# Performance work log

Measured on AMD Instinct MI355X. Metric: run time of the kernel, lower is better.

Reference implementation:

```python
import jax, jax.numpy as jnp
import numpy as np

B, S, HID, NH, NS = 2, 1024, 2048, 16, 8
D = HID // NH  # head_dim = 128


def setup_inputs() -> dict:
    key = jax.random.key(0)
    ks = jax.random.split(key, 8)
    inv = 1.0 / np.sqrt(HID)
    return {
        "hidden_states": jax.random.normal(ks[0], (B, S, HID), jnp.float32),
        "Wq": jax.random.normal(ks[1], (HID, HID), jnp.float32) * inv,
        "Wk": jax.random.normal(ks[2], (HID, HID), jnp.float32) * inv,
        "Wv": jax.random.normal(ks[3], (HID, HID), jnp.float32) * inv,
        "Wo": jax.random.normal(ks[4], (HID, HID), jnp.float32) * inv,
        "splat_positions": jax.random.normal(ks[5], (NH, NS, D), jnp.float32) * 0.02,
        "splat_directions": jax.random.normal(ks[6], (NH, NS, D), jnp.float32) * 0.02,
        "splat_log_scales": jnp.full((NH, NS), np.log(0.8), jnp.float32),
        "splat_log_amplitudes": jnp.full((NH, NS), -np.log(float(NS)), jnp.float32),
        "directional_strength": jnp.float32(0.3),
        "gsa_strength": jnp.float32(-6.0),
    }


def _affinities(tokens, positions, directions, scales, dir_strength):
    # tokens [B,NH,S,D]; positions/directions [NH,NS,D]; scales [NH,NS]
    tok_sq = jnp.sum(tokens * tokens, axis=-1)                       # [B,NH,S]
    pos_sq = jnp.sum(positions * positions, axis=-1)                 # [NH,NS]
    tp = jnp.einsum('bhsd,hnd->bhsn', tokens, positions)             # [B,NH,S,NS]
    dist2 = tok_sq[..., None] - 2.0 * tp + pos_sq[None, :, None, :]
    dist2 = jnp.maximum(dist2, 0.0)
    # signed projection of (token - position) onto unit direction
    proj = (jnp.einsum('bhsd,hnd->bhsn', tokens, directions)
            - jnp.sum(positions * directions, axis=-1)[None, :, None, :])
    perp2 = jnp.maximum(dist2 - proj * proj, 0.0)
    inv2s2 = (0.5 / (scales * scales))[None, :, None, :]
    radial = jnp.exp(-dist2 * inv2s2)
    directional = jnp.exp(-perp2 * inv2s2)
    return (1.0 - dir_strength) * radial + dir_strength * directional


def reference(hidden_states, Wq, Wk, Wv, Wo, splat_positions, splat_directions,
              splat_log_scales, splat_log_amplitudes, directional_strength, gsa_strength):
    b, s, hid = hidden_states.shape

    def heads(x):  # [B,S,HID] -> [B,NH,S,D]
        return x.reshape(b, s, NH, D).transpose(0, 2, 1, 3)

    q = heads(hidden_states @ Wq)
    k = heads(hidden_states @ Wk)
    v = heads(hidden_states @ Wv)

    # --- standard (original) attention path ---
    scores = jnp.einsum('bhqd,bhkd->bhqk', q, k) / jnp.sqrt(jnp.float32(D))
    attn = jax.nn.softmax(scores, axis=-1)
    std = jnp.einsum('bhqk,bhkd->bhqd', attn, v)
    std = std.transpose(0, 2, 1, 3).reshape(b, s, hid) @ Wo

    # --- directional GSA path ---
    eps = 1e-12
    positions = splat_positions / (jnp.linalg.norm(splat_positions, axis=-1, keepdims=True) + eps)
    positions = positions * (np.sqrt(D) * 0.3)
    directions = splat_directions / (jnp.linalg.norm(splat_directions, axis=-1, keepdims=True) + eps)
    scales = jnp.clip(jnp.exp(splat_log_scales), 0.3, 1.2)
    amplitudes = jax.nn.softmax(splat_log_amplitudes, axis=-1)
    ds = jax.nn.sigmoid(directional_strength)

    qa = _affinities(q, positions, directions, scales, ds)  # [B,NH,S,NS]
    ka = _affinities(k, positions, directions, scales, ds)  # [B,NH,S,NS]
    w = jnp.einsum('bhqn,hn,bhkn->bhqk', qa, amplitudes, ka)
    w = w / (jnp.sum(w, axis=-1, keepdims=True) + 1e-8)
    dgsa = jnp.einsum('bhqk,bhkd->bhqd', w, v)
    dgsa = dgsa.transpose(0, 2, 1, 3).reshape(b, s, hid) @ Wo

    gsa = jax.nn.sigmoid(gsa_strength)
    blend = jnp.minimum(0.05, gsa * 0.1)
    return (1.0 - blend) * std + blend * dgsa
```

## Files before the change

kernel.cpp:

```cpp
#include <hip/hip_runtime.h>
#include <math.h>

typedef __attribute__((ext_vector_type(8))) short bf16x8;
typedef __attribute__((ext_vector_type(4))) float f32x4;
typedef unsigned short ushort_t;

#define SQRT_D 11.313708498984761f
#define INV_SQRT_D 0.08838834764831845f

__device__ __forceinline__ unsigned short f2b(float f) {
    unsigned u = __float_as_uint(f);
    unsigned r = (u + 0x7fffu + ((u >> 16) & 1u)) >> 16;
    return (unsigned short)r;
}
__device__ __forceinline__ float b2f(unsigned short h) {
    return __uint_as_float(((unsigned)h) << 16);
}

__device__ __forceinline__ void async_copy16(const void* g, void* l) {
    __builtin_amdgcn_global_load_lds((const __attribute__((address_space(1))) void*)g,
                                     (__attribute__((address_space(3))) void*)l, 16, 0, 0);
}

__global__ __launch_bounds__(256) void prep(
    const float* __restrict__ X, const float* __restrict__ W0,
    const float* __restrict__ W1, const float* __restrict__ W2,
    const float* __restrict__ W3, const float* __restrict__ sp,
    const float* __restrict__ sd, const float* __restrict__ ls,
    const float* __restrict__ la, ushort_t* __restrict__ Xbf,
    ushort_t* __restrict__ WT4, float* __restrict__ posn,
    float* __restrict__ dirn, float* __restrict__ pos_sq,
    float* __restrict__ pdv, float* __restrict__ iv2s2,
    float* __restrict__ amp) {
    __shared__ float t[32][33];
    const int z = blockIdx.z;
    if (z < 4) {
        const float* W = (z == 0) ? W0 : (z == 1) ? W1 : (z == 2) ? W2 : W3;
        ushort_t* WT = WT4 + (size_t)z * 4194304;
        int tx = threadIdx.x & 31, ty = threadIdx.x >> 5;
        int bn = blockIdx.x * 32, bk = blockIdx.y * 32;
#pragma unroll
        for (int i = 0; i < 4; ++i)
            t[ty + i * 8][tx] = W[(size_t)(bk + ty + i * 8) * 2048 + bn + tx];
        __syncthreads();
#pragma unroll
        for (int i = 0; i < 4; ++i)
            WT[(size_t)(bn + ty + i * 8) * 2048 + bk + tx] = f2b(t[tx][ty + i * 8]);
        return;
    }
    {
        int bi = blockIdx.y * 64 + blockIdx.x;
        int i = (bi * 256 + threadIdx.x) * 4;
        float4 v = *(const float4*)(X + i);
        ushort4 o;
        o.x = f2b(v.x); o.y = f2b(v.y); o.z = f2b(v.z); o.w = f2b(v.w);
        *(ushort4*)(Xbf + i) = o;
    }
    if (blockIdx.x == 0 && blockIdx.y == 0 && threadIdx.x < 128) {
        int i = threadIdx.x;
        const float* p = sp + (size_t)i * 128;
        const float* d = sd + (size_t)i * 128;
        float np_ = 0.f, nd_ = 0.f;
        for (int k = 0; k < 128; ++k) { np_ += p[k] * p[k]; nd_ += d[k] * d[k]; }
        np_ = sqrtf(np_); nd_ = sqrtf(nd_);
        const float sc = 3.394112549695428f;
        float rp = sc / (np_ + 1e-12f);
        float rd = 1.f / (nd_ + 1e-12f);
        float psq = 0.f, pd_ = 0.f;
        for (int k = 0; k < 128; ++k) {
            float pn = p[k] * rp;
            float dn = d[k] * rd;
            posn[(size_t)i * 128 + k] = pn;
            dirn[(size_t)i * 128 + k] = dn;
            psq += pn * pn;
            pd_ += pn * dn;
        }
        pos_sq[i] = psq;
        pdv[i] = pd_;
        float s = expf(ls[i]);
        s = fminf(fmaxf(s, 0.3f), 1.2f);
        iv2s2[i] = 0.5f / (s * s);
        if ((i & 7) == 0) {
            int h = i >> 3;
            float mx = -INFINITY;
            for (int n = 0; n < 8; ++n) mx = fmaxf(mx, la[h * 8 + n]);
            float e[8]; float ssum = 0.f;
            for (int n = 0; n < 8; ++n) { e[n] = expf(la[h * 8 + n] - mx); ssum += e[n]; }
            for (int n = 0; n < 8; ++n) amp[h * 8 + n] = e[n] / ssum;
        }
    }
}


__global__ __launch_bounds__(256) void gemm_qkv(const ushort_t* __restrict__ A,
                                                const ushort_t* __restrict__ WT4,
                                                ushort_t* __restrict__ Qb,
                                                ushort_t* __restrict__ Kb,
                                                ushort_t* __restrict__ Vb,
                                                ushort_t* __restrict__ Vt) {
    __shared__ ushort_t As0[128 * 32], As1[128 * 32];
    __shared__ ushort_t Bs0[128 * 32], Bs1[128 * 32];
    const int tid = threadIdx.x, lane = tid & 63, wave = tid >> 6;
    const int l15 = lane & 15, quad = lane >> 4;
    const int wm = (wave >> 1) * 64, wn = (wave & 1) * 64;
    const int bm = blockIdx.x * 128;
    const int by = blockIdx.y, which = by >> 4, bn = (by & 15) * 128;
    const ushort_t* BT = WT4 + (size_t)which * 4194304;
    f32x4 acc[4][4] = {};
    const int off0 = tid * 16;
    const int row0 = tid >> 2;
    const int c0 = (tid & 3) ^ ((row0 + (row0 >> 2)) & 3);
    const ushort_t* ga = A + (size_t)(bm + row0) * 2048 + c0 * 8;
    const ushort_t* gb = BT + (size_t)(bn + row0) * 2048 + c0 * 8;
    const int rsw = (l15 + (l15 >> 2)) & 3;
#define STAGEG(ABUF, BBUF, k_)                                                 \
    {                                                                          \
        async_copy16(ga + (k_), (char*)(ABUF) + off0);                         \
        async_copy16(ga + (size_t)64 * 2048 + (k_), (char*)(ABUF) + off0 + 4096); \
        async_copy16(gb + (k_), (char*)(BBUF) + off0);                         \
        async_copy16(gb + (size_t)64 * 2048 + (k_), (char*)(BBUF) + off0 + 4096); \
    }
#define COMPUTEG(ABUF, BBUF)                                                   \
    {                                                                          \
        bf16x8 af[4], bfr[4];                                                  \
        _Pragma("unroll") for (int i = 0; i < 4; ++i)                          \
            af[i] = *(const bf16x8*)((const char*)(ABUF) + (wm + i * 16 + l15) * 64 + ((quad ^ rsw) << 4)); \
        _Pragma("unroll") for (int j = 0; j < 4; ++j)                          \
            bfr[j] = *(const bf16x8*)((const char*)(BBUF) + (wn + j * 16 + l15) * 64 + ((quad ^ rsw) << 4)); \
        _Pragma("unroll") for (int i = 0; i < 4; ++i)                          \
            _Pragma("unroll") for (int j = 0; j < 4; ++j)                      \
                acc[i][j] = __builtin_amdgcn_mfma_f32_16x16x32_bf16(af[i], bfr[j], acc[i][j], 0, 0, 0); \
    }
    STAGEG(As0, Bs0, 0);
    for (int k0 = 0; k0 < 2048; k0 += 64) {
        __syncthreads();
        STAGEG(As1, Bs1, k0 + 32);
        COMPUTEG(As0, Bs0);
        __syncthreads();
        if (k0 + 64 < 2048) STAGEG(As0, Bs0, k0 + 64);
        COMPUTEG(As1, Bs1);
    }
#undef STAGEG
#undef COMPUTEG
    ushort_t* Cb = (which == 0) ? Qb : ((which == 1) ? Kb : Vb);
    const bool dot = (which == 2);
    const float oscale = (which == 0) ? INV_SQRT_D : 1.f;
#pragma unroll
    for (int i = 0; i < 4; ++i) {
#pragma unroll
        for (int j = 0; j < 4; ++j) {
            int m0 = bm + wm + i * 16 + quad * 4;
            int n = bn + wn + j * 16 + l15;
            int b = m0 >> 10, s0 = m0 & 1023, h = n >> 7, d = n & 127;
            ushort4 pack;
            unsigned short* pp = (unsigned short*)&pack;
#pragma unroll
            for (int r = 0; r < 4; ++r) {
                unsigned short bv = f2b(acc[i][j][r] * oscale);
                pp[r] = bv;
                Cb[((size_t)((b << 4) | h) * 1024 + (s0 + r)) * 128 + d] = bv;
            }
            if (dot) *(ushort4*)(Vt + ((size_t)((b << 4) | h) * 128 + d) * 1024 + s0) = pack;
        }
    }
}

__global__ __launch_bounds__(256) void gemm_out(const ushort_t* __restrict__ A,
                                                const ushort_t* __restrict__ BT,
                                                float* __restrict__ Cf) {
    __shared__ ushort_t As0[128 * 32], As1[128 * 32];
    __shared__ ushort_t Bs0[64 * 32], Bs1[64 * 32];
    const int tid = threadIdx.x, lane = tid & 63, wave = tid >> 6;
    const int l15 = lane & 15, quad = lane >> 4;
    const int wm = (wave >> 1) * 64, wn = (wave & 1) * 32;
    const int bm = blockIdx.x * 128, bn = blockIdx.y * 64;
    f32x4 acc[4][2] = {};
    const int off0 = tid * 16;
    const int row0 = tid >> 2;
    const int c0 = (tid & 3) ^ ((row0 + (row0 >> 2)) & 3);
    const ushort_t* ga = A + (size_t)(bm + row0) * 2048 + c0 * 8;
    const ushort_t* gb = BT + (size_t)(bn + row0) * 2048 + c0 * 8;
    const int rsw = (l15 + (l15 >> 2)) & 3;
#define STAGEO(ABUF, BBUF, k_)                                                 \
    {                                                                          \
        async_copy16(ga + (k_), (char*)(ABUF) + off0);                         \
        async_copy16(ga + (size_t)64 * 2048 + (k_), (char*)(ABUF) + off0 + 4096); \
        async_copy16(gb + (k_), (char*)(BBUF) + off0);                         \
    }
#define COMPUTEO(ABUF, BBUF)                                                   \
    {                                                                          \
        bf16x8 af[4], bfr[2];                                                  \
        _Pragma("unroll") for (int i = 0; i < 4; ++i)                          \
            af[i] = *(const bf16x8*)((const char*)(ABUF) + (wm + i * 16 + l15) * 64 + ((quad ^ rsw) << 4)); \
        _Pragma("unroll") for (int j = 0; j < 2; ++j)                          \
            bfr[j] = *(const bf16x8*)((const char*)(BBUF) + (wn + j * 16 + l15) * 64 + ((quad ^ rsw) << 4)); \
        _Pragma("unroll") for (int i = 0; i < 4; ++i)                          \
            _Pragma("unroll") for (int j = 0; j < 2; ++j)                      \
                acc[i][j] = __builtin_amdgcn_mfma_f32_16x16x32_bf16(af[i], bfr[j], acc[i][j], 0, 0, 0); \
    }
    STAGEO(As0, Bs0, 0);
    for (int k0 = 0; k0 < 2048; k0 += 64) {
        __syncthreads();
        STAGEO(As1, Bs1, k0 + 32);
        COMPUTEO(As0, Bs0);
        __syncthreads();
        if (k0 + 64 < 2048) STAGEO(As0, Bs0, k0 + 64);
        COMPUTEO(As1, Bs1);
    }
#undef STAGEO
#undef COMPUTEO
#pragma unroll
    for (int i = 0; i < 4; ++i)
#pragma unroll
        for (int j = 0; j < 2; ++j)
#pragma unroll
            for (int r = 0; r < 4; ++r) {
                int m = bm + wm + i * 16 + quad * 4 + r;
                int n = bn + wn + j * 16 + l15;
                Cf[(size_t)m * 2048 + n] = acc[i][j][r];
            }
}

__global__ __launch_bounds__(256) void affinity_q(
    const ushort_t* __restrict__ Q,
    const float* __restrict__ posn, const float* __restrict__ dirn,
    const float* __restrict__ pos_sq, const float* __restrict__ pdv,
    const float* __restrict__ iv2s2, const float* __restrict__ ds_in,
    float* __restrict__ qa) {
    int gid = blockIdx.x * 256 + threadIdx.x;
    int n = gid & 7;
    int t = gid >> 3;
    const ushort_t* T = Q + (size_t)t * 128;
    int h = (t >> 10) & 15;
    const float* P = posn + (size_t)(h * 8 + n) * 128;
    const float* Dr = dirn + (size_t)(h * 8 + n) * 128;
    float tsq = 0.f, tp = 0.f, td = 0.f;
#pragma unroll
    for (int d = 0; d < 128; d += 8) {
        uint4 raw = *(const uint4*)(T + d);
        float tv[8];
        tv[0] = __uint_as_float(raw.x << 16); tv[1] = __uint_as_float(raw.x & 0xffff0000u);
        tv[2] = __uint_as_float(raw.y << 16); tv[3] = __uint_as_float(raw.y & 0xffff0000u);
        tv[4] = __uint_as_float(raw.z << 16); tv[5] = __uint_as_float(raw.z & 0xffff0000u);
        tv[6] = __uint_as_float(raw.w << 16); tv[7] = __uint_as_float(raw.w & 0xffff0000u);
        float4 p0 = *(const float4*)(P + d), p1 = *(const float4*)(P + d + 4);
        float4 d0 = *(const float4*)(Dr + d), d1 = *(const float4*)(Dr + d + 4);
        tsq += tv[0]*tv[0]+tv[1]*tv[1]+tv[2]*tv[2]+tv[3]*tv[3]+tv[4]*tv[4]+tv[5]*tv[5]+tv[6]*tv[6]+tv[7]*tv[7];
        tp  += tv[0]*p0.x+tv[1]*p0.y+tv[2]*p0.z+tv[3]*p0.w+tv[4]*p1.x+tv[5]*p1.y+tv[6]*p1.z+tv[7]*p1.w;
        td  += tv[0]*d0.x+tv[1]*d0.y+tv[2]*d0.z+tv[3]*d0.w+tv[4]*d1.x+tv[5]*d1.y+tv[6]*d1.z+tv[7]*d1.w;
    }
    const float fs = SQRT_D;
    tsq *= fs * fs; tp *= fs; td *= fs;
    float dist2 = fmaxf(tsq - 2.f * tp + pos_sq[h * 8 + n], 0.f);
    float proj = td - pdv[h * 8 + n];
    float perp2 = fmaxf(dist2 - proj * proj, 0.f);
    float iv = iv2s2[h * 8 + n];
    float dsv = 1.f / (1.f + __expf(-ds_in[0]));
    float aff = (1.f - dsv) * __expf(-dist2 * iv) + dsv * __expf(-perp2 * iv);
    qa[(size_t)t * 8 + n] = aff;
}

__global__ __launch_bounds__(128) void kv_s1_part(
    const ushort_t* __restrict__ K, const ushort_t* __restrict__ V,
    const float* __restrict__ posn, const float* __restrict__ dirn,
    const float* __restrict__ pos_sq, const float* __restrict__ pdv,
    const float* __restrict__ iv2s2, const float* __restrict__ ds_in,
    float* __restrict__ KVp, float* __restrict__ S1p) {
    __shared__ float kas[64][8];
    int bh = blockIdx.x, sc = blockIdx.y;
    int tid = threadIdx.x;
    int h = bh & 15;
    if (tid < 64) {
        const ushort_t* T = K + ((size_t)bh * 1024 + sc * 64 + tid) * 128;
        float tsq = 0.f, tp[8] = {}, td[8] = {};
        for (int d = 0; d < 128; d += 4) {
            uint2 raw = *(const uint2*)(T + d);
            float t0 = __uint_as_float(raw.x << 16), t1 = __uint_as_float(raw.x & 0xffff0000u);
            float t2 = __uint_as_float(raw.y << 16), t3 = __uint_as_float(raw.y & 0xffff0000u);
            tsq += t0 * t0 + t1 * t1 + t2 * t2 + t3 * t3;
#pragma unroll
            for (int n = 0; n < 8; ++n) {
                const float* P = posn + (size_t)(h * 8 + n) * 128 + d;
                const float* Dr = dirn + (size_t)(h * 8 + n) * 128 + d;
                tp[n] += t0 * P[0] + t1 * P[1] + t2 * P[2] + t3 * P[3];
                td[n] += t0 * Dr[0] + t1 * Dr[1] + t2 * Dr[2] + t3 * Dr[3];
            }
        }
        float dsv = 1.f / (1.f + __expf(-ds_in[0]));
#pragma unroll
        for (int n = 0; n < 8; ++n) {
            float dist2 = fmaxf(tsq - 2.f * tp[n] + pos_sq[h * 8 + n], 0.f);
            float proj = td[n] - pdv[h * 8 + n];
            float perp2 = fmaxf(dist2 - proj * proj, 0.f);
            float iv = iv2s2[h * 8 + n];
            kas[tid][n] = (1.f - dsv) * __expf(-dist2 * iv) + dsv * __expf(-perp2 * iv);
        }
    }
    __syncthreads();
    int d = tid;
    const ushort_t* VB = V + ((size_t)bh * 1024 + sc * 64) * 128;
    float acc[8] = {};
#pragma unroll 4
    for (int s = 0; s < 64; ++s) {
        float vd = b2f(VB[(size_t)s * 128 + d]);
#pragma unroll
        for (int n = 0; n < 8; ++n) acc[n] += kas[s][n] * vd;
    }
#pragma unroll
    for (int n = 0; n < 8; ++n) KVp[(((size_t)bh * 8 + n) * 16 + sc) * 128 + d] = acc[n];
    __shared__ float s1p[128];
    {
        int n = d >> 4, chunk = d & 15;
        float p = 0.f;
        for (int s = chunk * 4; s < chunk * 4 + 4; ++s) p += kas[s][n];
        s1p[d] = p;
    }
    __syncthreads();
    if (d < 8) {
        float t = 0.f;
        for (int c = 0; c < 16; ++c) t += s1p[(d << 4) + c];
        S1p[((size_t)bh * 8 + d) * 16 + sc] = t;
    }
}

__global__ __launch_bounds__(256) void flash_blend(
    const ushort_t* __restrict__ Qg, const ushort_t* __restrict__ Kg,
    const ushort_t* __restrict__ Vtg,
    const float* __restrict__ qa, const float* __restrict__ amp,
    const float* __restrict__ S1p, const float* __restrict__ KVp,
    const float* __restrict__ gstr, ushort_t* __restrict__ blended) {
    __shared__ ushort_t Ks0[64 * 128], Ks1[64 * 128];
    __shared__ ushort_t Vt0[128 * 64], Vt1[128 * 64];
    __shared__ ushort_t Ps[4][16 * 72];
    __shared__ float KVs[8 * 128];
    __shared__ float S1s[8];
    const int tid = threadIdx.x, lane = tid & 63, wave = tid >> 6;
    const int l15 = lane & 15, quad = lane >> 4;
    const int bh = blockIdx.y, qt = blockIdx.x;

    const ushort_t* Qrow = Qg + ((size_t)(bh * 1024 + qt * 64 + wave * 16 + l15)) * 128 + quad * 8;
    bf16x8 aq[4];
#pragma unroll
    for (int k4 = 0; k4 < 4; ++k4) aq[k4] = *(const bf16x8*)(Qrow + k4 * 32);

    {
        int n = tid >> 5, d = (tid & 31) * 4;
        f32x4 kv = {};
#pragma unroll
        for (int sc = 0; sc < 16; ++sc)
            kv += *(const f32x4*)(KVp + (((size_t)bh * 8 + n) * 16 + sc) * 128 + d);
        *(f32x4*)(KVs + tid * 4) = kv;
    }
    if (tid < 8) {
        float s = 0.f;
#pragma unroll
        for (int sc = 0; sc < 16; ++sc) s += S1p[((size_t)bh * 8 + tid) * 16 + sc];
        S1s[tid] = s;
    }

    const ushort_t* Kbase = Kg + (size_t)bh * 131072;
    const ushort_t* Vbase = Vtg + (size_t)bh * 131072;

#define STAGE(KBUF, VBUF, kt_)                                                        \
    {                                                                                 \
        _Pragma("unroll") for (int i_ = 0; i_ < 4; ++i_) {                            \
            int off_ = tid * 16 + i_ * 4096;                                          \
            int kr_ = off_ >> 8, kp_ = (off_ >> 4) & 15;                              \
            async_copy16(Kbase + (size_t)(kt_)*8192 + kr_ * 128 + ((kp_ ^ (kr_ & 15)) << 3), \
                         (char*)(KBUF) + off_);                                       \
            int vd_ = off_ >> 7, vp_ = (off_ >> 4) & 7;                               \
            async_copy16(Vbase + (size_t)vd_ * 1024 + (kt_)*64 + ((vp_ ^ (vd_ & 7)) << 3), \
                         (char*)(VBUF) + off_);                                       \
        }                                                                             \
    }
#define FLASH_STEP(KBUF, VBUF)                                                        \
    {                                                                                 \
        f32x4 sc[4] = {};                                                             \
        _Pragma("unroll") for (int k4 = 0; k4 < 4; ++k4) {                            \
            _Pragma("unroll") for (int t = 0; t < 4; ++t) {                           \
                bf16x8 bk = *(const bf16x8*)((const char*)(KBUF) +                    \
                                             ((t * 16 + l15) << 8) + (((k4 * 4 + quad) ^ l15) << 4)); \
                sc[t] = __builtin_amdgcn_mfma_f32_16x16x32_bf16(aq[k4], bk, sc[t], 0, 0, 0); \
            }                                                                         \
        }                                                                             \
        _Pragma("unroll") for (int t = 0; t < 4; ++t) {                               \
            _Pragma("unroll") for (int r = 0; r < 4; ++r) {                           \
                float p = __expf(sc[t][r]);                                           \
                l_i[r] += p;                                                          \
                Pw[(quad * 4 + r) * 72 + t * 16 + l15] = f2b(p);                      \
            }                                                                         \
        }                                                                             \
        bf16x8 ap0 = *(const bf16x8*)((const char*)Pw + (l15 * 72 + quad * 8) * 2);   \
        bf16x8 ap1 = *(const bf16x8*)((const char*)Pw + (l15 * 72 + 32 + quad * 8) * 2); \
        _Pragma("unroll") for (int j = 0; j < 8; ++j) {                               \
            bf16x8 bv0 = *(const bf16x8*)((const char*)(VBUF) +                       \
                                          ((j * 16 + l15) << 7) + (((quad) ^ (l15 & 7)) << 4)); \
            bf16x8 bv1 = *(const bf16x8*)((const char*)(VBUF) +                       \
                                          ((j * 16 + l15) << 7) + (((4 + quad) ^ (l15 & 7)) << 4)); \
            o[j] = __builtin_amdgcn_mfma_f32_16x16x32_bf16(ap0, bv0, o[j], 0, 0, 0);  \
            o[j] = __builtin_amdgcn_mfma_f32_16x16x32_bf16(ap1, bv1, o[j], 0, 0, 0);  \
        }                                                                             \
    }

    STAGE(Ks0, Vt0, 0);

    f32x4 o[8] = {};
    float l_i[4] = {};
    ushort_t* Pw = &Ps[wave][0];

    for (int kt = 0; kt < 16; kt += 2) {
        __syncthreads();
        STAGE(Ks1, Vt1, kt + 1);
        FLASH_STEP(Ks0, Vt0);
        __syncthreads();
        if (kt + 2 < 16) STAGE(Ks0, Vt0, kt + 2);
        FLASH_STEP(Ks1, Vt1);
    }
#undef STAGE
#undef FLASH_STEP
#pragma unroll
    for (int r = 0; r < 4; ++r) {
        float l = l_i[r];
        l += __shfl_xor(l, 1);
        l += __shfl_xor(l, 2);
        l += __shfl_xor(l, 4);
        l += __shfl_xor(l, 8);
        l_i[r] = l;
    }
    float gsa = 1.f / (1.f + __expf(-gstr[0]));
    float blend = fminf(0.05f, gsa * 0.1f);
    int b = bh >> 4, h = bh & 15;
#pragma unroll
    for (int r = 0; r < 4; ++r) {
        int q = qt * 64 + wave * 16 + quad * 4 + r;
        const float* qaRow = qa + ((size_t)bh * 1024 + q) * 8;
        float qam[8], Z = 0.f;
#pragma unroll
        for (int n = 0; n < 8; ++n) {
            qam[n] = qaRow[n] * amp[h * 8 + n];
            Z += qam[n] * S1s[n];
        }
        float invZ = 1.f / (Z + 1e-8f);
        float invl = 1.f / l_i[r];
        ushort_t* outp = blended + ((size_t)(b * 1024 + q)) * 2048 + h * 128;
#pragma unroll
        for (int j = 0; j < 8; ++j) {
            int d = j * 16 + l15;
            float dg = 0.f;
#pragma unroll
            for (int n = 0; n < 8; ++n) dg += qam[n] * KVs[n * 128 + d];
            float v = (1.f - blend) * (o[j][r] * invl) + blend * (dg * invZ);
            outp[d] = f2b(v);
        }
    }
}

extern "C" void kernel_launch(void* const* d_in, const int* in_sizes, int n_in,
                              void* d_out, int out_size, void* d_ws, size_t ws_size,
                              hipStream_t stream) {
    const float* X = (const float*)d_in[0];
    const float* Wq = (const float*)d_in[1];
    const float* Wk = (const float*)d_in[2];
    const float* Wv = (const float*)d_in[3];
    const float* Wo = (const float*)d_in[4];
    const float* sp = (const float*)d_in[5];
    const float* sd = (const float*)d_in[6];
    const float* ls = (const float*)d_in[7];
    const float* la = (const float*)d_in[8];
    const float* dstr = (const float*)d_in[9];
    const float* gstr = (const float*)d_in[10];

    char* base = (char*)d_ws;
    ushort_t* WT4 = (ushort_t*)base;      base += 33554432;
    ushort_t* Xbf = (ushort_t*)base;      base += 8388608;
    ushort_t* blended = Xbf;
    ushort_t* Qbf = (ushort_t*)base;      base += 8388608;
    ushort_t* Kbf = (ushort_t*)base;      base += 8388608;
    ushort_t* Vbf = (ushort_t*)base;      base += 8388608;
    ushort_t* Vtb = (ushort_t*)base;      base += 8388608;
    float* qaw = (float*)base;            base += 1048576;
    float* posn = (float*)base;           base += 65536;
    float* dirn = (float*)base;           base += 65536;
    float* pos_sq = (float*)base;         base += 512;
    float* pdv = (float*)base;            base += 512;
    float* iv2s2 = (float*)base;          base += 512;
    float* ampw = (float*)base;           base += 512;
    float* S1p = (float*)base;            base += 16384;
    float* KVp = (float*)base;            base += 2097152;

    prep<<<dim3(64, 64, 5), 256, 0, stream>>>(X, Wq, Wk, Wv, Wo, sp, sd, ls, la,
                                              Xbf, WT4, posn, dirn, pos_sq, pdv, iv2s2, ampw);
    gemm_qkv<<<dim3(16, 48), 256, 0, stream>>>(Xbf, WT4, Qbf, Kbf, Vbf, Vtb);
    affinity_q<<<1024, 256, 0, stream>>>(Qbf, posn, dirn, pos_sq, pdv, iv2s2, dstr, qaw);
    kv_s1_part<<<dim3(32, 16), 128, 0, stream>>>(Kbf, Vbf, posn, dirn, pos_sq, pdv, iv2s2,
                                                 dstr, KVp, S1p);
    flash_blend<<<dim3(16, 32), 256, 0, stream>>>(Qbf, Kbf, Vtb, qaw, ampw, S1p, KVp,
                                                  gstr, blended);
    gemm_out<<<dim3(16, 32), 256, 0, stream>>>(blended, WT4 + 12582912, (float*)d_out);
}
```

Baseline: 332.5 us.

## Restructure QKV GEMM into 256x256 tiles with four-stage async LDS pipeline

The QKV projection GEMM moves from 128x128 tiles with 256 threads and double buffering to 256x256 tiles with 512 threads (8 waves). It uses a four-slot LDS ring fed by async global-to-LDS loads, with explicit vmcnt waits, raw s_barrier, sched_barrier and setprio around the MFMA bursts. The larger tile raises arithmetic intensity per LDS byte and the deeper pipeline is meant to hide global load latency. In exchange it uses 128KB of LDS and a larger accumulator footprint. It also launches only 192 blocks, which may underfill the GPU.

```diff
diff --git a/kernel.cpp b/kernel.cpp
--- a/kernel.cpp
+++ b/kernel.cpp
@@ -92,75 +92,136 @@
 }
 
 
-__global__ __launch_bounds__(256) void gemm_qkv(const ushort_t* __restrict__ A,
-                                                const ushort_t* __restrict__ WT4,
-                                                ushort_t* __restrict__ Qb,
-                                                ushort_t* __restrict__ Kb,
-                                                ushort_t* __restrict__ Vb,
-                                                ushort_t* __restrict__ Vt) {
-    __shared__ ushort_t As0[128 * 32], As1[128 * 32];
-    __shared__ ushort_t Bs0[128 * 32], Bs1[128 * 32];
+__global__ __launch_bounds__(512, 2) void gemm_qkv(const ushort_t* __restrict__ A,
+                                                   const ushort_t* __restrict__ WT4,
+                                                   ushort_t* __restrict__ Qb,
+                                                   ushort_t* __restrict__ Kb,
+                                                   ushort_t* __restrict__ Vb,
+                                                   ushort_t* __restrict__ Vt) {
+    __shared__ ushort_t Asl[4 * 8192];
+    __shared__ ushort_t Bsl[4 * 8192];
     const int tid = threadIdx.x, lane = tid & 63, wave = tid >> 6;
     const int l15 = lane & 15, quad = lane >> 4;
-    const int wm = (wave >> 1) * 64, wn = (wave & 1) * 64;
-    const int bm = blockIdx.x * 128;
-    const int by = blockIdx.y, which = by >> 4, bn = (by & 15) * 128;
+    const int wr = wave >> 2, wc = wave & 3;
+    const int wm = wr * 128, wn = wc * 64;
+    const int bm = blockIdx.x * 256;
+    const int by = blockIdx.y, which = by >> 3, bn = (by & 7) * 256;
     const ushort_t* BT = WT4 + (size_t)which * 4194304;
-    f32x4 acc[4][4] = {};
-    const int off0 = tid * 16;
-    const int row0 = tid >> 2;
-    const int c0 = (tid & 3) ^ ((row0 + (row0 >> 2)) & 3);
-    const ushort_t* ga = A + (size_t)(bm + row0) * 2048 + c0 * 8;
-    const ushort_t* gb = BT + (size_t)(bn + row0) * 2048 + c0 * 8;
+    f32x4 acc[8][4] = {};
+    const int srow = tid >> 2;
+    const int sc = tid & 3;
+    const int swz0 = (srow + (srow >> 2)) & 3;
+    const ushort_t* gA = A + (size_t)(bm + srow) * 2048 + (sc ^ swz0) * 8;
+    const ushort_t* gB = BT + (size_t)(bn + srow) * 2048 + (sc ^ swz0) * 8;
+    char* ldsA = (char*)Asl + tid * 16;
+    char* ldsB = (char*)Bsl + tid * 16;
     const int rsw = (l15 + (l15 >> 2)) & 3;
-#define STAGEG(ABUF, BBUF, k_)                                                 \
+    const int cxo = (quad ^ rsw) << 4;
+    bf16x8 bfr[4];
+
+#define STAGE_A(slot, kofs)                                                    \
     {                                                                          \
-        async_copy16(ga + (k_), (char*)(ABUF) + off0);                         \
-        async_copy16(ga + (size_t)64 * 2048 + (k_), (char*)(ABUF) + off0 + 4096); \
-        async_copy16(gb + (k_), (char*)(BBUF) + off0);                         \
-        async_copy16(gb + (size_t)64 * 2048 + (k_), (char*)(BBUF) + off0 + 4096); \
-    }
-#define COMPUTEG(ABUF, BBUF)                                                   \
+        char* db_ = ldsA + (slot) * 16384;                                     \
+        async_copy16(gA + (kofs), db_);                                        \
+        async_copy16(gA + 262144 + (kofs), db_ + 8192);                        \
+    }
+#define STAGE_B(slot, kofs)                                                    \
     {                                                                          \
-        bf16x8 af[4], bfr[4];                                                  \
+        char* db_ = ldsB + (slot) * 16384;                                     \
+        async_copy16(gB + (kofs), db_);                                        \
+        async_copy16(gB + 262144 + (kofs), db_ + 8192);                        \
+    }
+#define VMW(n) asm volatile("s_waitcnt vmcnt(" #n ")" ::: "memory")
+#define PHA(sa, ISSUE, WAIT)                                                   \
+    {                                                                          \
+        const char* Ab_ = (const char*)Asl + (sa) * 16384;                     \
+        const char* Bb_ = (const char*)Bsl + (sa) * 16384;                     \
+        bf16x8 af[4];                                                          \
         _Pragma("unroll") for (int i = 0; i < 4; ++i)                          \
-            af[i] = *(const bf16x8*)((const char*)(ABUF) + (wm + i * 16 + l15) * 64 + ((quad ^ rsw) << 4)); \
+            af[i] = *(const bf16x8*)(Ab_ + (wm + i * 16 + l15) * 64 + cxo);    \
         _Pragma("unroll") for (int j = 0; j < 4; ++j)                          \
-            bfr[j] = *(const bf16x8*)((const char*)(BBUF) + (wn + j * 16 + l15) * 64 + ((quad ^ rsw) << 4)); \
+            bfr[j] = *(const bf16x8*)(Bb_ + (wn + j * 16 + l15) * 64 + cxo);   \
+        ISSUE;                                                                 \
+        WAIT;                                                                  \
+        __builtin_amdgcn_s_barrier();                                          \
+        asm volatile("s_waitcnt lgkmcnt(0)" ::: "memory");                     \
+        __builtin_amdgcn_sched_barrier(0);                                     \
+        __builtin_amdgcn_s_setprio(1);                                         \
         _Pragma("unroll") for (int i = 0; i < 4; ++i)                          \
             _Pragma("unroll") for (int j = 0; j < 4; ++j)                      \
                 acc[i][j] = __builtin_amdgcn_mfma_f32_16x16x32_bf16(af[i], bfr[j], acc[i][j], 0, 0, 0); \
-    }
-    STAGEG(As0, Bs0, 0);
-    for (int k0 = 0; k0 < 2048; k0 += 64) {
-        __syncthreads();
-        STAGEG(As1, Bs1, k0 + 32);
-        COMPUTEG(As0, Bs0);
-        __syncthreads();
-        if (k0 + 64 < 2048) STAGEG(As0, Bs0, k0 + 64);
-        COMPUTEG(As1, Bs1);
-    }
-#undef STAGEG
-#undef COMPUTEG
+        __builtin_amdgcn_s_setprio(0);                                         \
+        __builtin_amdgcn_s_barrier();                                          \
+    }
+#define PHB(sa, ISSUE, WAIT)                                                   \
+    {                                                                          \
+        const char* Ab_ = (const char*)Asl + (sa) * 16384;                     \
+        bf16x8 af[4];                                                          \
+        _Pragma("unroll") for (int i = 0; i < 4; ++i)                          \
+            af[i] = *(const bf16x8*)(Ab_ + (wm + (i + 4) * 16 + l15) * 64 + cxo); \
+        ISSUE;                                                                 \
+        WAIT;                                                                  \
+        __builtin_amdgcn_s_barrier();                                          \
+        asm volatile("s_waitcnt lgkmcnt(0)" ::: "memory");                     \
+        __builtin_amdgcn_sched_barrier(0);                                     \
+        __builtin_amdgcn_s_setprio(1);                                         \
+        _Pragma("unroll") for (int i = 0; i < 4; ++i)                          \
+            _Pragma("unroll") for (int j = 0; j < 4; ++j)                      \
+                acc[i + 4][j] = __builtin_amdgcn_mfma_f32_16x16x32_bf16(af[i], bfr[j], acc[i + 4][j], 0, 0, 0); \
+        __builtin_amdgcn_s_setprio(0);                                         \
+        __builtin_amdgcn_s_barrier();                                          \
+    }
+
+    STAGE_A(0, 0);
+    STAGE_B(0, 0);
+    STAGE_A(1, 32);
+    STAGE_B(1, 32);
+    STAGE_A(2, 64);
+    STAGE_B(2, 64);
+    VMW(8);
+    __builtin_amdgcn_s_barrier();
+
+#pragma unroll 2
+    for (int t = 0; t < 30; ++t) {
+        const int s0 = (2 * t) & 3;
+        PHA(s0, STAGE_A(s0 ^ 3, (t + 1) * 64 + 32), );
+        PHB(s0, STAGE_B(s0 ^ 3, (t + 1) * 64 + 32), VMW(8));
+        PHA(s0 + 1, STAGE_A(s0, (t + 2) * 64), );
+        PHB(s0 + 1, STAGE_B(s0, (t + 2) * 64), VMW(8));
+    }
+    PHA(0, STAGE_A(3, 31 * 64 + 32), );
+    PHB(0, STAGE_B(3, 31 * 64 + 32), VMW(8));
+    PHA(1, , );
+    PHB(1, , VMW(4));
+    PHA(2, , );
+    PHB(2, , VMW(0));
+    PHA(3, , );
+    PHB(3, , );
+#undef STAGE_A
+#undef STAGE_B
+#undef VMW
+#undef PHA
+#undef PHB
+
     ushort_t* Cb = (which == 0) ? Qb : ((which == 1) ? Kb : Vb);
     const bool dot = (which == 2);
     const float oscale = (which == 0) ? INV_SQRT_D : 1.f;
 #pragma unroll
-    for (int i = 0; i < 4; ++i) {
+    for (int i = 0; i < 8; ++i) {
 #pragma unroll
         for (int j = 0; j < 4; ++j) {
             int m0 = bm + wm + i * 16 + quad * 4;
             int n = bn + wn + j * 16 + l15;
-            int b = m0 >> 10, s0 = m0 & 1023, h = n >> 7, d = n & 127;
+            int b = m0 >> 10, s0_ = m0 & 1023, h = n >> 7, d = n & 127;
             ushort4 pack;
             unsigned short* pp = (unsigned short*)&pack;
 #pragma unroll
             for (int r = 0; r < 4; ++r) {
                 unsigned short bv = f2b(acc[i][j][r] * oscale);
                 pp[r] = bv;
-                Cb[((size_t)((b << 4) | h) * 1024 + (s0 + r)) * 128 + d] = bv;
+                Cb[((size_t)((b << 4) | h) * 1024 + (s0_ + r)) * 128 + d] = bv;
             }
-            if (dot) *(ushort4*)(Vt + ((size_t)((b << 4) | h) * 128 + d) * 1024 + s0) = pack;
+            if (dot) *(ushort4*)(Vt + ((size_t)((b << 4) | h) * 128 + d) * 1024 + s0_) = pack;
         }
     }
 }
@@ -490,7 +551,7 @@
 
     prep<<<dim3(64, 64, 5), 256, 0, stream>>>(X, Wq, Wk, Wv, Wo, sp, sd, ls, la,
                                               Xbf, WT4, posn, dirn, pos_sq, pdv, iv2s2, ampw);
-    gemm_qkv<<<dim3(16, 48), 256, 0, stream>>>(Xbf, WT4, Qbf, Kbf, Vbf, Vtb);
+    gemm_qkv<<<dim3(8, 24), 512, 0, stream>>>(Xbf, WT4, Qbf, Kbf, Vbf, Vtb);
     affinity_q<<<1024, 256, 0, stream>>>(Qbf, posn, dirn, pos_sq, pdv, iv2s2, dstr, qaw);
     kv_s1_part<<<dim3(32, 16), 128, 0, stream>>>(Kbf, Vbf, posn, dirn, pos_sq, pdv, iv2s2,
                                                  dstr, KVp, S1p);
```

Result: no change. 333.7 us (+0.4%).
